# Kernel optimization log

Measured on AMD Instinct MI355X. Metric: run time of the kernel, lower is better.

## Reference

```python
import jax, jax.numpy as jnp
import numpy as np

N, HIDDEN, HEADS, HEAD = 20000, 128, 8, 16
LAP, NBUCKETS, NBINS, MAXDEG, E = 16, 1024, 32, 64, 320000


def _mlp(x, W1, b1, W2, b2):
    return jax.nn.relu(x @ W1 + b1) @ W2 + b2


def _build_pairs(bq, bk, edge_index):
    """Host-side: P_LSH = {(i,j)!=: bq[i]==bk[j]} union graph edges, deduped.
    Mirrors _lsh_pairs + torch.unique (data-dependent size -> numpy)."""
    bq = np.asarray(bq); bk = np.asarray(bk); ei = np.asarray(edge_index)
    srcs = [ei[0].astype(np.int64)]; dsts = [ei[1].astype(np.int64)]
    common = np.intersect1d(np.unique(bq), np.unique(bk))
    for b in common:
        qn = np.nonzero(bq == b)[0]
        kn = np.nonzero(bk == b)[0]
        ii = np.repeat(qn, kn.size)
        jj = np.tile(kn, qn.size)
        m = ii != jj
        srcs.append(ii[m].astype(np.int64)); dsts.append(jj[m].astype(np.int64))
    src = np.concatenate(srcs); dst = np.concatenate(dsts)
    code = np.unique(src * np.int64(N) + dst)  # dedup pairs
    return jnp.asarray(code // N, jnp.int32), jnp.asarray(code % N, jnp.int32)


def setup_inputs() -> dict:
    key = jax.random.key(0)
    ks = jax.random.split(key, 16)
    rn = lambda k, sh, s=1.0: (jax.random.normal(k, sh, jnp.float32) * s)
    d_in = HIDDEN + LAP
    return {
        "Q": rn(ks[0], (N, HIDDEN)),
        "K": rn(ks[1], (N, HIDDEN)),
        "V": rn(ks[2], (N, HIDDEN)),
        "lap_pe": jax.random.uniform(ks[3], (N, LAP), jnp.float32),
        "W_q1": rn(ks[4], (d_in, HIDDEN), d_in ** -0.5), "b_q1": jnp.zeros((HIDDEN,), jnp.float32),
        "W_q2": rn(ks[5], (HIDDEN, NBUCKETS), HIDDEN ** -0.5), "b_q2": jnp.zeros((NBUCKETS,), jnp.float32),
        "W_k1": rn(ks[6], (d_in, HIDDEN), d_in ** -0.5), "b_k1": jnp.zeros((HIDDEN,), jnp.float32),
        "W_k2": rn(ks[7], (HIDDEN, NBUCKETS), HIDDEN ** -0.5), "b_k2": jnp.zeros((NBUCKETS,), jnp.float32),
        "spd_bias": rn(ks[8], (NBINS + 1, HEADS), 0.02),
        "deg_src_emb": rn(ks[9], (MAXDEG + 2, HEADS), 0.02),
        "deg_dst_emb": rn(ks[10], (MAXDEG + 2, HEADS), 0.02),
        "W_out": rn(ks[11], (HIDDEN, HIDDEN), HIDDEN ** -0.5), "b_out": jnp.zeros((HIDDEN,), jnp.float32),
        "spd_boundaries": jnp.linspace(0.0, 2.0, NBINS).astype(jnp.float32),
        "edge_index": jax.random.randint(ks[12], (2, E), 0, N, jnp.int32),
        "deg": jax.random.randint(ks[13], (N,), 0, MAXDEG + 1, jnp.int32),
    }


def reference(Q, K, V, lap_pe, W_q1, b_q1, W_q2, b_q2, W_k1, b_k1, W_k2, b_k2,
              spd_bias, deg_src_emb, deg_dst_emb, W_out, b_out, spd_boundaries,
              edge_index, deg):
    q_in = jnp.concatenate([Q, lap_pe], axis=-1)
    k_in = jnp.concatenate([K, lap_pe], axis=-1)
    l_q = _mlp(q_in, W_q1, b_q1, W_q2, b_q2)  # (N, B)
    l_k = _mlp(k_in, W_k1, b_k1, W_k2, b_k2)
    src, dst = _build_pairs(jnp.argmax(l_q, -1), jnp.argmax(l_k, -1), edge_index)

    Qh = Q.reshape(N, HEADS, HEAD)
    Kh = K.reshape(N, HEADS, HEAD)
    Vh = V.reshape(N, HEADS, HEAD)

    scores = jnp.einsum("ehd,ehd->eh", Qh[src], Kh[dst]) / (HEAD ** 0.5)  # (P, H)
    pe_dist = jnp.linalg.norm(lap_pe[src] - lap_pe[dst], axis=-1)
    spd_idx = jnp.searchsorted(spd_boundaries, pe_dist, side="left")  # torch.bucketize(right=False)
    scores = scores + spd_bias[spd_idx]
    dsrc = jnp.clip(deg[src], 0, MAXDEG + 1)
    ddst = jnp.clip(deg[dst], 0, MAXDEG + 1)
    scores = scores + deg_src_emb[dsrc] + deg_dst_emb[ddst]

    # pyg_softmax: segment softmax over src index
    m = jax.ops.segment_max(scores, src, num_segments=N)  # (N, H)
    m = jnp.where(jnp.isneginf(m), 0.0, m)
    ex = jnp.exp(scores - m[src])
    denom = jax.ops.segment_sum(ex, src, num_segments=N)
    alpha = ex / (denom[src] + 1e-16)  # dropout p=0 (eval)

    h = jax.ops.segment_sum(alpha[..., None] * Vh[dst], src, num_segments=N)
    h_global = h.reshape(N, HIDDEN) @ W_out + b_out
    return h_global, l_q, l_k
```

## Files before the change

kernel.cpp:

```cpp
#include <hip/hip_runtime.h>
#include <math.h>

#define NN 20000
#define HID 128
#define NH 8
#define HD 16
#define LAPD 16
#define NB 1024
#define NBINS 32
#define MAXDEG 64
#define NE 320000
#define DIN 144

#define NEGH (-1.0e30f)

__global__ __launch_bounds__(256) void mlp_kernel(
    const float* __restrict__ X, const float* __restrict__ lap,
    const float* __restrict__ W1, const float* __restrict__ b1,
    const float* __restrict__ W2, const float* __restrict__ b2,
    float* __restrict__ outL, int* __restrict__ bidx)
{
    __shared__ __align__(16) float xs[16][DIN];
    __shared__ __align__(16) float hs[16][HID];
    __shared__ float rbv[64];
    __shared__ int   rbi[64];
    const int tid = threadIdx.x;
    const int n0 = blockIdx.x * 16;

    for (int e = tid; e < 16 * DIN; e += 256) {
        int n = e / DIN, k = e - n * DIN;
        float v = (k < HID) ? X[(size_t)(n0 + n) * HID + k]
                            : lap[(size_t)(n0 + n) * LAPD + (k - HID)];
        xs[n][k] = v;
    }
    __syncthreads();

    const int c = tid & 127, ng = tid >> 7;
    float hacc[8];
    {
        float bb = b1[c];
        #pragma unroll
        for (int m = 0; m < 8; m++) hacc[m] = bb;
        for (int k = 0; k < DIN; k += 4) {
            float w0 = W1[(k + 0) * HID + c];
            float w1 = W1[(k + 1) * HID + c];
            float w2 = W1[(k + 2) * HID + c];
            float w3 = W1[(k + 3) * HID + c];
            #pragma unroll
            for (int m = 0; m < 8; m++) {
                float4 xv = *(const float4*)&xs[ng * 8 + m][k];
                hacc[m] = fmaf(xv.x, w0, hacc[m]);
                hacc[m] = fmaf(xv.y, w1, hacc[m]);
                hacc[m] = fmaf(xv.z, w2, hacc[m]);
                hacc[m] = fmaf(xv.w, w3, hacc[m]);
            }
        }
    }
    #pragma unroll
    for (int m = 0; m < 8; m++) hs[ng * 8 + m][c] = fmaxf(hacc[m], 0.0f);
    __syncthreads();

    float a0[16], a1[16], a2[16], a3[16];
    #pragma unroll
    for (int m = 0; m < 16; m++) { a0[m] = 0.f; a1[m] = 0.f; a2[m] = 0.f; a3[m] = 0.f; }

    for (int k = 0; k < HID; k += 4) {
        const float4 w0 = *(const float4*)&W2[(size_t)(k + 0) * NB + 4 * tid];
        const float4 w1 = *(const float4*)&W2[(size_t)(k + 1) * NB + 4 * tid];
        const float4 w2 = *(const float4*)&W2[(size_t)(k + 2) * NB + 4 * tid];
        const float4 w3 = *(const float4*)&W2[(size_t)(k + 3) * NB + 4 * tid];
        #pragma unroll
        for (int m = 0; m < 16; m++) {
            const float4 hv = *(const float4*)&hs[m][k];
            a0[m] = fmaf(hv.x, w0.x, fmaf(hv.y, w1.x, fmaf(hv.z, w2.x, fmaf(hv.w, w3.x, a0[m]))));
            a1[m] = fmaf(hv.x, w0.y, fmaf(hv.y, w1.y, fmaf(hv.z, w2.y, fmaf(hv.w, w3.y, a1[m]))));
            a2[m] = fmaf(hv.x, w0.z, fmaf(hv.y, w1.z, fmaf(hv.z, w2.z, fmaf(hv.w, w3.z, a2[m]))));
            a3[m] = fmaf(hv.x, w0.w, fmaf(hv.y, w1.w, fmaf(hv.z, w2.w, fmaf(hv.w, w3.w, a3[m]))));
        }
    }

    const float4 bb4 = *(const float4*)&b2[4 * tid];
    const int lane = tid & 63, wv = tid >> 6;
    const int o0 = 4 * tid;
    for (int m = 0; m < 16; m++) {
        float4 ov;
        ov.x = a0[m] + bb4.x; ov.y = a1[m] + bb4.y;
        ov.z = a2[m] + bb4.z; ov.w = a3[m] + bb4.w;
        *(float4*)&outL[(size_t)(n0 + m) * NB + o0] = ov;
        float bv = ov.x; int bi = o0;
        if (ov.y > bv) { bv = ov.y; bi = o0 + 1; }
        if (ov.z > bv) { bv = ov.z; bi = o0 + 2; }
        if (ov.w > bv) { bv = ov.w; bi = o0 + 3; }
        #pragma unroll
        for (int off = 1; off < 64; off <<= 1) {
            float ovv = __shfl_xor(bv, off, 64);
            int   oi  = __shfl_xor(bi, off, 64);
            if (ovv > bv || (ovv == bv && oi < bi)) { bv = ovv; bi = oi; }
        }
        if (lane == 0) { rbv[wv * 16 + m] = bv; rbi[wv * 16 + m] = bi; }
    }
    __syncthreads();
    if (tid < 16) {
        float bv = rbv[tid]; int bi = rbi[tid];
        #pragma unroll
        for (int ww = 1; ww < 4; ww++) {
            float ov = rbv[ww * 16 + tid]; int oi = rbi[ww * 16 + tid];
            if (ov > bv || (ov == bv && oi < bi)) { bv = ov; bi = oi; }
        }
        bidx[n0 + tid] = min(max(bi, 0), NB - 1);
    }
}

__global__ void zero_kernel(int* __restrict__ p, int n) {
    int i = blockIdx.x * 256 + threadIdx.x;
    if (i < n) p[i] = 0;
}

__global__ void hist_kernel(const int* __restrict__ bkarr, int* __restrict__ bcnt) {
    int i = blockIdx.x * 256 + threadIdx.x;
    if (i < NN) {
        int b = min(max(bkarr[i], 0), NB - 1);
        atomicAdd(&bcnt[b], 1);
    }
}

__global__ __launch_bounds__(1024) void scan_bucket_kernel(const int* __restrict__ cnt,
        int* __restrict__ off, int* __restrict__ fill) {
    __shared__ int s[1024];
    int t = threadIdx.x;
    int v = cnt[t];
    s[t] = v; __syncthreads();
    for (int o = 1; o < 1024; o <<= 1) {
        int a = (t >= o) ? s[t - o] : 0;
        __syncthreads();
        s[t] += a;
        __syncthreads();
    }
    int excl = s[t] - v;
    off[t] = excl; fill[t] = excl;
    if (t == 1023) off[NB] = s[1023];
}

__global__ __launch_bounds__(1024) void scan_edge_kernel(const int* __restrict__ cnt,
        int* __restrict__ off, int* __restrict__ fill) {
    __shared__ int s[1024];
    const int t = threadIdx.x;
    const int base = t * 20;
    int loc[20]; int sum = 0;
    #pragma unroll
    for (int k = 0; k < 20; k++) {
        int idx = base + k;
        int v = (idx < NN) ? cnt[idx] : 0;
        loc[k] = sum; sum += v;
    }
    s[t] = sum; __syncthreads();
    for (int o = 1; o < 1024; o <<= 1) {
        int a = (t >= o) ? s[t - o] : 0;
        __syncthreads();
        s[t] += a;
        __syncthreads();
    }
    int pre = s[t] - sum;
    #pragma unroll
    for (int k = 0; k < 20; k++) {
        int idx = base + k;
        if (idx < NN) { int e = pre + loc[k]; off[idx] = e; fill[idx] = e; }
    }
    if (t == 1023) off[NN] = s[1023];
}

__global__ void scatter_bucket_kernel(const int* __restrict__ bkarr,
        int* __restrict__ fill, int* __restrict__ blist) {
    int i = blockIdx.x * 256 + threadIdx.x;
    if (i < NN) {
        int b = min(max(bkarr[i], 0), NB - 1);
        int p = atomicAdd(&fill[b], 1);
        if (p >= 0 && p < NN) blist[p] = i;
    }
}

__global__ void edge_count_kernel(const int* __restrict__ ei, int* __restrict__ ecnt) {
    int e = blockIdx.x * 256 + threadIdx.x;
    if (e < NE) {
        int s = min(max(ei[e], 0), NN - 1);
        atomicAdd(&ecnt[s], 1);
    }
}

__global__ void edge_scatter_kernel(const int* __restrict__ ei,
        int* __restrict__ fill, int* __restrict__ adj) {
    int e = blockIdx.x * 256 + threadIdx.x;
    if (e < NE) {
        int s = min(max(ei[e], 0), NN - 1);
        int d = min(max(ei[NE + e], 0), NN - 1);
        int p = atomicAdd(&fill[s], 1);
        if (p >= 0 && p < NE) adj[p] = d;
    }
}

__global__ __launch_bounds__(64, 4) void attn_kernel(
    const float* __restrict__ Q, const float* __restrict__ K, const float* __restrict__ V,
    const float* __restrict__ lap,
    const float* __restrict__ spdb, const float* __restrict__ dse,
    const float* __restrict__ dde, const float* __restrict__ bndr,
    const int* __restrict__ deg,
    const int* __restrict__ bq, const int* __restrict__ bkarr,
    const int* __restrict__ boff, const int* __restrict__ blist,
    const int* __restrict__ eoff, const int* __restrict__ adj,
    const float* __restrict__ Wout, const float* __restrict__ bout,
    float* __restrict__ outH)
{
    __shared__ __align__(16) float qf[128];
    __shared__ float pef[16];
    __shared__ float bnd[32];
    __shared__ int   jls[64];
    __shared__ float wtsT[8][65];
    __shared__ float al8[8];
    __shared__ float lsum[8];
    __shared__ float hsm[128];
    __shared__ float spdbs[(NBINS + 1) * NH];
    __shared__ float ddes[(MAXDEG + 2) * NH];
    const int i = blockIdx.x;
    const int lane = threadIdx.x;
    const int h0 = lane >> 4;
    const int h1 = h0 + 4;

    qf[lane]      = Q[(size_t)i * HID + lane];
    qf[lane + 64] = Q[(size_t)i * HID + 64 + lane];
    if (lane < 16) pef[lane] = lap[(size_t)i * LAPD + lane];
    if (lane < 32) bnd[lane] = bndr[lane];
    for (int e = lane; e < (NBINS + 1) * NH; e += 64) spdbs[e] = spdb[e];
    for (int e = lane; e < (MAXDEG + 2) * NH; e += 64) ddes[e] = dde[e];

    int b = min(max(bq[i], 0), NB - 1);
    int bs = boff[b], be = boff[b + 1];
    bs = min(max(bs, 0), NN); be = min(max(be, bs), NN);
    int es = eoff[i], ee = eoff[i + 1];
    es = min(max(es, 0), NE); ee = min(max(ee, es), NE);
    const int Lb = be - bs;
    const int Ltot = Lb + (ee - es);
    const int degi = min(max(deg[i], 0), MAXDEG + 1);
    __syncthreads();

    float dsrc[8];
    #pragma unroll
    for (int h = 0; h < 8; h++) dsrc[h] = dse[degi * 8 + h];

    float m8[8], l8[8];
    #pragma unroll
    for (int h = 0; h < 8; h++) { m8[h] = NEGH; l8[h] = 0.0f; }
    float acc0 = 0.0f, acc1 = 0.0f;

    for (int t0 = 0; t0 < Ltot; t0 += 64) {
        const int t = t0 + lane;
        int j = 0; bool valid = false;
        if (t < Ltot) {
            if (t < Lb) {
                j = blist[bs + t];
                j = min(max(j, 0), NN - 1);
                valid = (j != i);
            } else {
                const int p = t - Lb;
                j = adj[es + p];
                j = min(max(j, 0), NN - 1);
                valid = (j == i) || (bkarr[j] != b);
                if (valid) {
                    for (int q = 0; q < p; q++)
                        if (adj[es + q] == j) { valid = false; break; }
                }
            }
        }
        jls[lane] = valid ? j : 0;

        float s8[8];
        if (valid) {
            const float4* K4 = (const float4*)(K + (size_t)j * HID);
            #pragma unroll
            for (int h = 0; h < 8; h++) {
                float4 k0 = K4[h * 4 + 0], k1 = K4[h * 4 + 1];
                float4 k2 = K4[h * 4 + 2], k3 = K4[h * 4 + 3];
                float4 q0 = *(const float4*)&qf[h * 16 + 0];
                float4 q1 = *(const float4*)&qf[h * 16 + 4];
                float4 q2 = *(const float4*)&qf[h * 16 + 8];
                float4 q3 = *(const float4*)&qf[h * 16 + 12];
                float dot = 0.0f;
                dot = fmaf(q0.x, k0.x, dot); dot = fmaf(q0.y, k0.y, dot);
                dot = fmaf(q0.z, k0.z, dot); dot = fmaf(q0.w, k0.w, dot);
                dot = fmaf(q1.x, k1.x, dot); dot = fmaf(q1.y, k1.y, dot);
                dot = fmaf(q1.z, k1.z, dot); dot = fmaf(q1.w, k1.w, dot);
                dot = fmaf(q2.x, k2.x, dot); dot = fmaf(q2.y, k2.y, dot);
                dot = fmaf(q2.z, k2.z, dot); dot = fmaf(q2.w, k2.w, dot);
                dot = fmaf(q3.x, k3.x, dot); dot = fmaf(q3.y, k3.y, dot);
                dot = fmaf(q3.z, k3.z, dot); dot = fmaf(q3.w, k3.w, dot);
                s8[h] = dot * 0.25f;
            }
            const float* lj = lap + (size_t)j * LAPD;
            float ss = 0.0f;
            #pragma unroll
            for (int d = 0; d < 16; d++) { float df = pef[d] - lj[d]; ss = fmaf(df, df, ss); }
            float dist = sqrtf(ss);
            int si = 0;
            #pragma unroll
            for (int kb = 0; kb < 32; kb++) si += (bnd[kb] < dist) ? 1 : 0;
            const int dj = min(max(deg[j], 0), MAXDEG + 1);
            #pragma unroll
            for (int h = 0; h < 8; h++)
                s8[h] += spdbs[si * 8 + h] + dsrc[h] + ddes[dj * 8 + h];
        } else {
            #pragma unroll
            for (int h = 0; h < 8; h++) s8[h] = NEGH;
        }

        float alpha8[8];
        #pragma unroll
        for (int h = 0; h < 8; h++) {
            float cm = s8[h];
            #pragma unroll
            for (int off = 1; off < 64; off <<= 1)
                cm = fmaxf(cm, __shfl_xor(cm, off, 64));
            const float mn = fmaxf(m8[h], cm);
            alpha8[h] = __expf(m8[h] - mn);
            float p = valid ? __expf(s8[h] - mn) : 0.0f;
            float sp = p;
            #pragma unroll
            for (int off = 1; off < 64; off <<= 1)
                sp += __shfl_xor(sp, off, 64);
            l8[h] = l8[h] * alpha8[h] + sp;
            m8[h] = mn;
            wtsT[h][lane] = p;
        }
        if (lane == 0) {
            #pragma unroll
            for (int h = 0; h < 8; h++) al8[h] = alpha8[h];
        }
        __syncthreads();

        acc0 *= al8[h0];
        acc1 *= al8[h1];
        const int rem = Ltot - t0;
        const int nc = (rem >= 64) ? 64 : ((rem + 7) & ~7);
        #pragma unroll 8
        for (int cc = 0; cc < nc; ++cc) {
            const int jc = __builtin_amdgcn_readfirstlane(jls[cc]);
            const float w0 = wtsT[h0][cc];
            const float w1 = wtsT[h1][cc];
            const float* vr = V + (size_t)jc * HID;
            acc0 = fmaf(w0, vr[lane], acc0);
            acc1 = fmaf(w1, vr[lane + 64], acc1);
        }
        __syncthreads();
    }

    if (lane == 0) {
        #pragma unroll
        for (int h = 0; h < 8; h++) lsum[h] = l8[h];
    }
    __syncthreads();
    const float linv0 = 1.0f / (lsum[h0] + 1e-16f);
    const float linv1 = 1.0f / (lsum[h1] + 1e-16f);
    hsm[lane]      = acc0 * linv0;
    hsm[lane + 64] = acc1 * linv1;
    __syncthreads();

    float o0 = bout[lane];
    float o1 = bout[lane + 64];
    for (int k = 0; k < HID; k++) {
        const float hk = hsm[k];
        o0 = fmaf(hk, Wout[k * HID + lane], o0);
        o1 = fmaf(hk, Wout[k * HID + 64 + lane], o1);
    }
    outH[(size_t)i * HID + lane]      = o0;
    outH[(size_t)i * HID + 64 + lane] = o1;
}

extern "C" void kernel_launch(void* const* d_in, const int* in_sizes, int n_in,
                              void* d_out, int out_size, void* d_ws, size_t ws_size,
                              hipStream_t stream) {
    const float* Q    = (const float*)d_in[0];
    const float* Kx   = (const float*)d_in[1];
    const float* Vx   = (const float*)d_in[2];
    const float* lap  = (const float*)d_in[3];
    const float* Wq1  = (const float*)d_in[4];
    const float* bq1  = (const float*)d_in[5];
    const float* Wq2  = (const float*)d_in[6];
    const float* bq2  = (const float*)d_in[7];
    const float* Wk1  = (const float*)d_in[8];
    const float* bk1  = (const float*)d_in[9];
    const float* Wk2  = (const float*)d_in[10];
    const float* bk2  = (const float*)d_in[11];
    const float* spdb = (const float*)d_in[12];
    const float* dse  = (const float*)d_in[13];
    const float* dde  = (const float*)d_in[14];
    const float* Wout = (const float*)d_in[15];
    const float* bout = (const float*)d_in[16];
    const float* bndr = (const float*)d_in[17];
    const int*   ei   = (const int*)d_in[18];
    const int*   deg  = (const int*)d_in[19];

    float* out   = (float*)d_out;
    float* outH  = out;
    float* outLq = out + (size_t)NN * HID;
    float* outLk = outLq + (size_t)NN * NB;

    int* wsp = (int*)d_ws;
    size_t o = 0;
    auto carve = [&](size_t n_ints) -> int* {
        int* p = wsp + o; o += n_ints; return p;
    };
    int* bcnt  = carve(NB);
    int* boff  = carve(NB + 1);
    int* bfill = carve(NB);
    int* blist = carve(NN);
    int* bqv   = carve(NN);
    int* bkv   = carve(NN);
    int* ecnt  = carve(NN);
    int* eoff  = carve(NN + 1);
    int* efill = carve(NN);
    int* adj   = carve(NE);

    zero_kernel<<<(NB + 255) / 256, 256, 0, stream>>>(bcnt, NB);
    zero_kernel<<<(NN + 255) / 256, 256, 0, stream>>>(ecnt, NN);

    mlp_kernel<<<NN / 16, 256, 0, stream>>>(Q,  lap, Wq1, bq1, Wq2, bq2, outLq, bqv);
    mlp_kernel<<<NN / 16, 256, 0, stream>>>(Kx, lap, Wk1, bk1, Wk2, bk2, outLk, bkv);

    hist_kernel<<<(NN + 255) / 256, 256, 0, stream>>>(bkv, bcnt);
    scan_bucket_kernel<<<1, 1024, 0, stream>>>(bcnt, boff, bfill);
    scatter_bucket_kernel<<<(NN + 255) / 256, 256, 0, stream>>>(bkv, bfill, blist);

    edge_count_kernel<<<(NE + 255) / 256, 256, 0, stream>>>(ei, ecnt);
    scan_edge_kernel<<<1, 1024, 0, stream>>>(ecnt, eoff, efill);
    edge_scatter_kernel<<<(NE + 255) / 256, 256, 0, stream>>>(ei, efill, adj);

    attn_kernel<<<NN, 64, 0, stream>>>(Q, Kx, Vx, lap, spdb, dse, dde, bndr, deg,
                                       bqv, bkv, boff, blist, eoff, adj,
                                       Wout, bout, outH);
}
```

Measured before the change: 1.023 ms.

## Pre-dedup edges, sort queries by bucket, pack four waves per block

```diff
diff --git a/kernel.cpp b/kernel.cpp
--- a/kernel.cpp
+++ b/kernel.cpp
@@ -198,91 +198,129 @@
     }
 }
 
-__global__ __launch_bounds__(64, 4) void attn_kernel(
+__global__ __launch_bounds__(256) void dedup_kernel(
+    const int* __restrict__ eoff, int* __restrict__ adj,
+    const int* __restrict__ bqv, const int* __restrict__ bkv,
+    int* __restrict__ acnt)
+{
+    __shared__ int prev[4][192];
+    const int lane = threadIdx.x & 63, wv = threadIdx.x >> 6;
+    const int i = blockIdx.x * 4 + wv;
+    if (i >= NN) return;
+    int es = eoff[i], ee = eoff[i + 1];
+    es = min(max(es, 0), NE); ee = min(max(ee, es), NE);
+    const int d = ee - es;
+    const int b = min(max(bqv[i], 0), NB - 1);
+    int kept = 0;
+    for (int t0 = 0; t0 < d; t0 += 64) {
+        const int t = t0 + lane;
+        const bool in = t < d;
+        int j = -1;
+        if (in) j = min(max(adj[es + t], 0), NN - 1);
+        bool keep = in && ((j == i) || (bkv[j] != b));
+        const int nin = min(64, d - t0);
+        for (int q2 = 0; q2 < nin; q2++) {
+            int jq = __shfl(j, q2, 64);
+            if (in && q2 < lane && jq == j) keep = false;
+        }
+        if (t0 > 0 && in) {
+            asm volatile("s_waitcnt lgkmcnt(0)" ::: "memory");
+            const int np = min(t0, 192);
+            for (int q2 = 0; q2 < np; q2++)
+                if (prev[wv][q2] == j) keep = false;
+        }
+        if (in && t < 192) prev[wv][t] = j;
+        unsigned long long km = __ballot(keep);
+        int pos = __popcll(km & ((1ull << lane) - 1ull));
+        if (keep) adj[es + kept + pos] = j;
+        kept += (int)__popcll(km);
+    }
+    if (lane == 0) acnt[i] = kept;
+}
+
+__global__ __launch_bounds__(256, 3) void attn_kernel(
     const float* __restrict__ Q, const float* __restrict__ K, const float* __restrict__ V,
     const float* __restrict__ lap,
     const float* __restrict__ spdb, const float* __restrict__ dse,
     const float* __restrict__ dde, const float* __restrict__ bndr,
     const int* __restrict__ deg,
-    const int* __restrict__ bq, const int* __restrict__ bkarr,
+    const int* __restrict__ bq,
     const int* __restrict__ boff, const int* __restrict__ blist,
-    const int* __restrict__ eoff, const int* __restrict__ adj,
+    const int* __restrict__ eoff, const int* __restrict__ acnt,
+    const int* __restrict__ adj, const int* __restrict__ qlist,
     const float* __restrict__ Wout, const float* __restrict__ bout,
     float* __restrict__ outH)
 {
-    __shared__ __align__(16) float qf[128];
-    __shared__ float pef[16];
+    __shared__ __align__(16) float qfl[4][128];
+    __shared__ __align__(16) float pefl[4][16];
+    __shared__ __align__(16) float hsm[4][128];
+    __shared__ float wts[4][8][66];
+    __shared__ int   jls[4][64];
+    __shared__ __align__(16) float spdbs[(NBINS + 1) * NH];
+    __shared__ __align__(16) float ddes[(MAXDEG + 2) * NH];
     __shared__ float bnd[32];
-    __shared__ int   jls[64];
-    __shared__ float wtsT[8][65];
-    __shared__ float al8[8];
-    __shared__ float lsum[8];
-    __shared__ float hsm[128];
-    __shared__ float spdbs[(NBINS + 1) * NH];
-    __shared__ float ddes[(MAXDEG + 2) * NH];
-    const int i = blockIdx.x;
-    const int lane = threadIdx.x;
-    const int h0 = lane >> 4;
-    const int h1 = h0 + 4;
-
-    qf[lane]      = Q[(size_t)i * HID + lane];
-    qf[lane + 64] = Q[(size_t)i * HID + 64 + lane];
-    if (lane < 16) pef[lane] = lap[(size_t)i * LAPD + lane];
-    if (lane < 32) bnd[lane] = bndr[lane];
-    for (int e = lane; e < (NBINS + 1) * NH; e += 64) spdbs[e] = spdb[e];
-    for (int e = lane; e < (MAXDEG + 2) * NH; e += 64) ddes[e] = dde[e];
+
+    const int tid = threadIdx.x;
+    const int wv = tid >> 6, lane = tid & 63;
+    const int cq = lane >> 2, qq = lane & 3;
+
+    int blk = (int)blockIdx.x;
+    blk = (blk & 7) * 625 + (blk >> 3);
+    const int task = blk * 4 + wv;
+    int i = qlist[task];
+    i = min(max(i, 0), NN - 1);
+
+    for (int e = tid; e < (NBINS + 1) * NH; e += 256) spdbs[e] = spdb[e];
+    for (int e = tid; e < (MAXDEG + 2) * NH; e += 256) ddes[e] = dde[e];
+    if (tid < 32) bnd[tid] = bndr[tid];
+    qfl[wv][lane]      = Q[(size_t)i * HID + lane];
+    qfl[wv][lane + 64] = Q[(size_t)i * HID + 64 + lane];
+    if (lane < 16) pefl[wv][lane] = lap[(size_t)i * LAPD + lane];
 
     int b = min(max(bq[i], 0), NB - 1);
     int bs = boff[b], be = boff[b + 1];
     bs = min(max(bs, 0), NN); be = min(max(be, bs), NN);
-    int es = eoff[i], ee = eoff[i + 1];
-    es = min(max(es, 0), NE); ee = min(max(ee, es), NE);
+    int es = eoff[i];
+    es = min(max(es, 0), NE);
+    int na = min(max(acnt[i], 0), NE - es);
     const int Lb = be - bs;
-    const int Ltot = Lb + (ee - es);
+    const int Ltot = Lb + na;
     const int degi = min(max(deg[i], 0), MAXDEG + 1);
     __syncthreads();
 
-    float dsrc[8];
-    #pragma unroll
-    for (int h = 0; h < 8; h++) dsrc[h] = dse[degi * 8 + h];
+    const float4 ds0 = *(const float4*)&dse[degi * 8];
+    const float4 ds1 = *(const float4*)&dse[degi * 8 + 4];
 
     float m8[8], l8[8];
     #pragma unroll
     for (int h = 0; h < 8; h++) { m8[h] = NEGH; l8[h] = 0.0f; }
-    float acc0 = 0.0f, acc1 = 0.0f;
+    float acc[32];
+    #pragma unroll
+    for (int k = 0; k < 32; k++) acc[k] = 0.0f;
 
     for (int t0 = 0; t0 < Ltot; t0 += 64) {
         const int t = t0 + lane;
-        int j = 0; bool valid = false;
+        int j = i; bool valid = false;
         if (t < Ltot) {
             if (t < Lb) {
-                j = blist[bs + t];
-                j = min(max(j, 0), NN - 1);
+                j = min(max(blist[bs + t], 0), NN - 1);
                 valid = (j != i);
             } else {
-                const int p = t - Lb;
-                j = adj[es + p];
-                j = min(max(j, 0), NN - 1);
-                valid = (j == i) || (bkarr[j] != b);
-                if (valid) {
-                    for (int q = 0; q < p; q++)
-                        if (adj[es + q] == j) { valid = false; break; }
-                }
+                j = min(max(adj[es + (t - Lb)], 0), NN - 1);
+                valid = true;
             }
         }
-        jls[lane] = valid ? j : 0;
 
         float s8[8];
         if (valid) {
             const float4* K4 = (const float4*)(K + (size_t)j * HID);
+            const float4* Q4 = (const float4*)&qfl[wv][0];
             #pragma unroll
             for (int h = 0; h < 8; h++) {
                 float4 k0 = K4[h * 4 + 0], k1 = K4[h * 4 + 1];
                 float4 k2 = K4[h * 4 + 2], k3 = K4[h * 4 + 3];
-                float4 q0 = *(const float4*)&qf[h * 16 + 0];
-                float4 q1 = *(const float4*)&qf[h * 16 + 4];
-                float4 q2 = *(const float4*)&qf[h * 16 + 8];
-                float4 q3 = *(const float4*)&qf[h * 16 + 12];
+                float4 q0 = Q4[h * 4 + 0], q1 = Q4[h * 4 + 1];
+                float4 q2 = Q4[h * 4 + 2], q3 = Q4[h * 4 + 3];
                 float dot = 0.0f;
                 dot = fmaf(q0.x, k0.x, dot); dot = fmaf(q0.y, k0.y, dot);
                 dot = fmaf(q0.z, k0.z, dot); dot = fmaf(q0.w, k0.w, dot);
@@ -294,18 +332,30 @@
                 dot = fmaf(q3.z, k3.z, dot); dot = fmaf(q3.w, k3.w, dot);
                 s8[h] = dot * 0.25f;
             }
-            const float* lj = lap + (size_t)j * LAPD;
+            const float4* P4 = (const float4*)&pefl[wv][0];
+            const float4* L4 = (const float4*)(lap + (size_t)j * LAPD);
             float ss = 0.0f;
             #pragma unroll
-            for (int d = 0; d < 16; d++) { float df = pef[d] - lj[d]; ss = fmaf(df, df, ss); }
+            for (int d4 = 0; d4 < 4; d4++) {
+                float4 pe = P4[d4], lj = L4[d4];
+                float dx = pe.x - lj.x, dy = pe.y - lj.y;
+                float dz = pe.z - lj.z, dw = pe.w - lj.w;
+                ss = fmaf(dx, dx, ss); ss = fmaf(dy, dy, ss);
+                ss = fmaf(dz, dz, ss); ss = fmaf(dw, dw, ss);
+            }
             float dist = sqrtf(ss);
             int si = 0;
             #pragma unroll
             for (int kb = 0; kb < 32; kb++) si += (bnd[kb] < dist) ? 1 : 0;
             const int dj = min(max(deg[j], 0), MAXDEG + 1);
-            #pragma unroll
-            for (int h = 0; h < 8; h++)
-                s8[h] += spdbs[si * 8 + h] + dsrc[h] + ddes[dj * 8 + h];
+            const float4 sb0 = *(const float4*)&spdbs[si * 8];
+            const float4 sb1 = *(const float4*)&spdbs[si * 8 + 4];
+            const float4 db0 = *(const float4*)&ddes[dj * 8];
+            const float4 db1 = *(const float4*)&ddes[dj * 8 + 4];
+            s8[0] += sb0.x + ds0.x + db0.x; s8[1] += sb0.y + ds0.y + db0.y;
+            s8[2] += sb0.z + ds0.z + db0.z; s8[3] += sb0.w + ds0.w + db0.w;
+            s8[4] += sb1.x + ds1.x + db1.x; s8[5] += sb1.y + ds1.y + db1.y;
+            s8[6] += sb1.z + ds1.z + db1.z; s8[7] += sb1.w + ds1.w + db1.w;
         } else {
             #pragma unroll
             for (int h = 0; h < 8; h++) s8[h] = NEGH;
@@ -320,52 +370,91 @@
                 cm = fmaxf(cm, __shfl_xor(cm, off, 64));
             const float mn = fmaxf(m8[h], cm);
             alpha8[h] = __expf(m8[h] - mn);
-            float p = valid ? __expf(s8[h] - mn) : 0.0f;
-            float sp = p;
-            #pragma unroll
-            for (int off = 1; off < 64; off <<= 1)
-                sp += __shfl_xor(sp, off, 64);
-            l8[h] = l8[h] * alpha8[h] + sp;
+            const float p = valid ? __expf(s8[h] - mn) : 0.0f;
+            l8[h] = l8[h] * alpha8[h] + p;
             m8[h] = mn;
-            wtsT[h][lane] = p;
-        }
-        if (lane == 0) {
-            #pragma unroll
-            for (int h = 0; h < 8; h++) al8[h] = alpha8[h];
-        }
-        __syncthreads();
-
-        acc0 *= al8[h0];
-        acc1 *= al8[h1];
+            wts[wv][h][lane] = p;
+        }
+        jls[wv][lane] = valid ? j : i;
+
+        float aq0, aq1;
+        if (qq == 0)      { aq0 = alpha8[0]; aq1 = alpha8[1]; }
+        else if (qq == 1) { aq0 = alpha8[2]; aq1 = alpha8[3]; }
+        else if (qq == 2) { aq0 = alpha8[4]; aq1 = alpha8[5]; }
+        else              { aq0 = alpha8[6]; aq1 = alpha8[7]; }
+
+        #pragma unroll
+        for (int k = 0; k < 16; k++) acc[k] *= aq0;
+        #pragma unroll
+        for (int k = 16; k < 32; k++) acc[k] *= aq1;
+
+        asm volatile("s_waitcnt lgkmcnt(0)" ::: "memory");
+
         const int rem = Ltot - t0;
-        const int nc = (rem >= 64) ? 64 : ((rem + 7) & ~7);
-        #pragma unroll 8
-        for (int cc = 0; cc < nc; ++cc) {
-            const int jc = __builtin_amdgcn_readfirstlane(jls[cc]);
-            const float w0 = wtsT[h0][cc];
-            const float w1 = wtsT[h1][cc];
-            const float* vr = V + (size_t)jc * HID;
-            acc0 = fmaf(w0, vr[lane], acc0);
-            acc1 = fmaf(w1, vr[lane + 64], acc1);
-        }
-        __syncthreads();
-    }
-
-    if (lane == 0) {
-        #pragma unroll
-        for (int h = 0; h < 8; h++) lsum[h] = l8[h];
-    }
-    __syncthreads();
-    const float linv0 = 1.0f / (lsum[h0] + 1e-16f);
-    const float linv1 = 1.0f / (lsum[h1] + 1e-16f);
-    hsm[lane]      = acc0 * linv0;
-    hsm[lane + 64] = acc1 * linv1;
-    __syncthreads();
+        const int npass = ((rem < 64 ? rem : 64) + 15) >> 4;
+        for (int r = 0; r < npass; r++) {
+            const int cc = r * 16 + cq;
+            const int jc = jls[wv][cc];
+            const float w0 = wts[wv][2 * qq][cc];
+            const float w1 = wts[wv][2 * qq + 1][cc];
+            const float4* V4 = (const float4*)(V + (size_t)jc * HID + qq * 32);
+            #pragma unroll
+            for (int s = 0; s < 4; s++) {
+                const float4 v = V4[s];
+                acc[s * 4 + 0] = fmaf(w0, v.x, acc[s * 4 + 0]);
+                acc[s * 4 + 1] = fmaf(w0, v.y, acc[s * 4 + 1]);
+                acc[s * 4 + 2] = fmaf(w0, v.z, acc[s * 4 + 2]);
+                acc[s * 4 + 3] = fmaf(w0, v.w, acc[s * 4 + 3]);
+            }
+            #pragma unroll
+            for (int s = 4; s < 8; s++) {
+                const float4 v = V4[s];
+                acc[s * 4 + 0] = fmaf(w1, v.x, acc[s * 4 + 0]);
+                acc[s * 4 + 1] = fmaf(w1, v.y, acc[s * 4 + 1]);
+                acc[s * 4 + 2] = fmaf(w1, v.z, acc[s * 4 + 2]);
+                acc[s * 4 + 3] = fmaf(w1, v.w, acc[s * 4 + 3]);
+            }
+        }
+    }
+
+    #pragma unroll
+    for (int h = 0; h < 8; h++) {
+        float v = l8[h];
+        #pragma unroll
+        for (int off = 1; off < 64; off <<= 1) v += __shfl_xor(v, off, 64);
+        l8[h] = v;
+    }
+    float lq0, lq1;
+    if (qq == 0)      { lq0 = l8[0]; lq1 = l8[1]; }
+    else if (qq == 1) { lq0 = l8[2]; lq1 = l8[3]; }
+    else if (qq == 2) { lq0 = l8[4]; lq1 = l8[5]; }
+    else              { lq0 = l8[6]; lq1 = l8[7]; }
+    const float linv0 = 1.0f / (lq0 + 1e-16f);
+    const float linv1 = 1.0f / (lq1 + 1e-16f);
+    #pragma unroll
+    for (int k = 0; k < 16; k++) acc[k] *= linv0;
+    #pragma unroll
+    for (int k = 16; k < 32; k++) acc[k] *= linv1;
+
+    #pragma unroll
+    for (int k = 0; k < 32; k++) {
+        float v = acc[k];
+        v += __shfl_xor(v, 4, 64);
+        v += __shfl_xor(v, 8, 64);
+        v += __shfl_xor(v, 16, 64);
+        v += __shfl_xor(v, 32, 64);
+        acc[k] = v;
+    }
+    if (cq == 0) {
+        #pragma unroll
+        for (int k = 0; k < 32; k++) hsm[wv][qq * 32 + k] = acc[k];
+    }
+    asm volatile("s_waitcnt lgkmcnt(0)" ::: "memory");
 
     float o0 = bout[lane];
     float o1 = bout[lane + 64];
     for (int k = 0; k < HID; k++) {
-        const float hk = hsm[k];
+        const float hk = hsm[wv][k];
         o0 = fmaf(hk, Wout[k * HID + lane], o0);
         o1 = fmaf(hk, Wout[k * HID + 64 + lane], o1);
     }
@@ -417,6 +506,8 @@
     int* eoff  = carve(NN + 1);
     int* efill = carve(NN);
     int* adj   = carve(NE);
+    int* qoff  = carve(NB + 1);
+    int* qlist = carve(NN);
 
     zero_kernel<<<(NB + 255) / 256, 256, 0, stream>>>(bcnt, NB);
     zero_kernel<<<(NN + 255) / 256, 256, 0, stream>>>(ecnt, NN);
@@ -428,11 +519,18 @@
     scan_bucket_kernel<<<1, 1024, 0, stream>>>(bcnt, boff, bfill);
     scatter_bucket_kernel<<<(NN + 255) / 256, 256, 0, stream>>>(bkv, bfill, blist);
 
+    zero_kernel<<<(NB + 255) / 256, 256, 0, stream>>>(bcnt, NB);
+    hist_kernel<<<(NN + 255) / 256, 256, 0, stream>>>(bqv, bcnt);
+    scan_bucket_kernel<<<1, 1024, 0, stream>>>(bcnt, qoff, bfill);
+    scatter_bucket_kernel<<<(NN + 255) / 256, 256, 0, stream>>>(bqv, bfill, qlist);
+
     edge_count_kernel<<<(NE + 255) / 256, 256, 0, stream>>>(ei, ecnt);
     scan_edge_kernel<<<1, 1024, 0, stream>>>(ecnt, eoff, efill);
     edge_scatter_kernel<<<(NE + 255) / 256, 256, 0, stream>>>(ei, efill, adj);
 
-    attn_kernel<<<NN, 64, 0, stream>>>(Q, Kx, Vx, lap, spdb, dse, dde, bndr, deg,
-                                       bqv, bkv, boff, blist, eoff, adj,
-                                       Wout, bout, outH);
-}
+    dedup_kernel<<<NN / 4, 256, 0, stream>>>(eoff, adj, bqv, bkv, ecnt);
+
+    attn_kernel<<<NN / 4, 256, 0, stream>>>(Q, Kx, Vx, lap, spdb, dse, dde, bndr, deg,
+                                            bqv, boff, blist, eoff, ecnt, adj, qlist,
+                                            Wout, bout, outH);
+}
```

Result: faster. 882.6 us (-13.7%).
